# Optimization experiments

Measured on AMD Instinct MI355X. Metric: run time of the kernel, lower is better.

The kernel has to match this reference:

```python
import jax, jax.numpy as jnp
import numpy as np

NUM_HEADS = 16

def _apply_rope(t, cos, sin):
    # t: [B, nh, S, hd]; cos/sin: [S, hd//2]
    t1 = t[..., 0::2]
    t2 = t[..., 1::2]
    c = cos[None, None, :, :]
    s = sin[None, None, :, :]
    r1 = t1 * c - t2 * s
    r2 = t1 * s + t2 * c
    # interleave back to [..., hd]
    out = jnp.stack([r1, r2], axis=-1)
    return out.reshape(t.shape)

def setup_inputs() -> dict:
    key = jax.random.key(0)
    ks = jax.random.split(key, 6)
    B, S, H = 1, 4096, 1024
    hd = H // NUM_HEADS
    x = jax.random.normal(ks[0], (B, S, H), dtype=jnp.float32)
    # RoPE angle matrix: theta[pos, i] = pos / 10000^(2i/hd), shape [context, hd//2]
    pos = jnp.arange(S, dtype=jnp.float32)[:, None]
    inv_freq = 1.0 / (10000.0 ** (jnp.arange(0, hd, 2, dtype=jnp.float32) / hd))
    rotation = pos * inv_freq[None, :]
    sc = 1.0 / np.sqrt(H)
    W_qkv = jax.random.normal(ks[1], (H, 3 * H), dtype=jnp.float32) * sc
    b_qkv = jax.random.normal(ks[2], (3 * H,), dtype=jnp.float32) * 0.01
    W_out = jax.random.normal(ks[3], (H, H), dtype=jnp.float32) * sc
    b_out = jax.random.normal(ks[4], (H,), dtype=jnp.float32) * 0.01
    return {"x": x, "rotation": rotation, "W_qkv": W_qkv, "b_qkv": b_qkv,
            "W_out": W_out, "b_out": b_out, "window_size": 33}

def reference(x, rotation, W_qkv, b_qkv, W_out, b_out, window_size):
    B, S, H = x.shape
    nh = NUM_HEADS
    hd = H // nh
    W = window_size
    pad = W // 2
    qkv = x @ W_qkv + b_qkv                               # [B, S, 3H]
    qkv = qkv.reshape(B, S, nh, 3 * hd).transpose(0, 2, 1, 3)  # [B, nh, S, 3hd]
    q, k, v = jnp.split(qkv, 3, axis=-1)                  # each [B, nh, S, hd]
    cos = jnp.cos(rotation[:S])
    sin = jnp.sin(rotation[:S])
    q = _apply_rope(q, cos, sin)
    k = _apply_rope(k, cos, sin)
    # zero-pad along sequence, then gather sliding windows
    k_pad = jnp.pad(k, ((0, 0), (0, 0), (pad, pad), (0, 0)))
    v_pad = jnp.pad(v, ((0, 0), (0, 0), (pad, pad), (0, 0)))
    idx = jnp.arange(S)[:, None] + jnp.arange(W)[None, :]  # [S, W]
    k_win = k_pad[:, :, idx, :]                            # [B, nh, S, W, hd]
    v_win = v_pad[:, :, idx, :]
    scores = jnp.einsum('bnsh,bnswh->bnsw', q, k_win) / np.sqrt(hd)
    attn = jax.nn.softmax(scores, axis=-1)
    ctx = jnp.einsum('bnsw,bnswh->bnsh', attn, v_win)      # [B, nh, S, hd]
    ctx = ctx.transpose(0, 2, 1, 3).reshape(B, S, H)
    return ctx @ W_out + b_out
```

## Files before the change

kernel.cpp:

```cpp
#include <hip/hip_runtime.h>
#include <hip/hip_bf16.h>

#define S_LEN 4096
#define NH 16
#define HD 64
#define WIN 33
#define PAD 16
#define QT 64
#define KROWS 96
#define KPITCH_U 36

typedef short short8 __attribute__((ext_vector_type(8)));
typedef float f32x4 __attribute__((ext_vector_type(4)));

__device__ __forceinline__ float bl(unsigned u){ return __uint_as_float(u << 16); }
__device__ __forceinline__ float bh(unsigned u){ return __uint_as_float(u & 0xffff0000u); }
__device__ __forceinline__ unsigned f2bfu(float f){
  unsigned u = __float_as_uint(f);
  return (u + 0x7fffu + ((u >> 16) & 1u)) >> 16;
}
__device__ __forceinline__ unsigned pack2(float a, float b){ return f2bfu(a) | (f2bfu(b) << 16); }

__device__ __forceinline__ void gload_lds16(const void* g, void* l){
  __builtin_amdgcn_global_load_lds(
      (const __attribute__((address_space(1))) void*)g,
      (__attribute__((address_space(3))) void*)l, 16, 0, 0);
}


__global__ __launch_bounds__(256) void prep_all(
    const float* __restrict__ rot, float2* __restrict__ csq,
    const float* __restrict__ x, __hip_bfloat16* __restrict__ xb,
    const float* __restrict__ Wq, __hip_bfloat16* __restrict__ Wt1,
    const float* __restrict__ Wo, __hip_bfloat16* __restrict__ Wt2,
    const float* __restrict__ b_out, float* __restrict__ out)
{
  __shared__ float tile[32][33];
  const int b = blockIdx.x, tid = threadIdx.x;
  if (b < 512) {
    int t = b * 256 + tid;
    float v = rot[t], sv, cv;
    __sincosf(v, &sv, &cv);
    csq[t] = make_float2(cv, sv);
  } else if (b < 2560) {
    int t = (b - 512) * 256 + tid;
    const float4* p = (const float4*)x + (size_t)t * 2;
    float4 a = p[0], c = p[1];
    uint4 o;
    o.x = pack2(a.x, a.y); o.y = pack2(a.z, a.w);
    o.z = pack2(c.x, c.y); o.w = pack2(c.z, c.w);
    ((uint4*)xb)[t] = o;
  } else if (b < 6656) {
    const float* in; unsigned short* outp; int R, C, bx, by;
    if (b < 5632) { int bb = b - 2560; in = Wq; outp = (unsigned short*)Wt1; R = 1024; C = 3072; bx = bb % 96; by = bb / 96; }
    else          { int bb = b - 5632; in = Wo; outp = (unsigned short*)Wt2; R = 1024; C = 1024; bx = bb % 32; by = bb / 32; }
    int c0 = bx * 32, r0 = by * 32;
    int tx = tid & 31, ty = tid >> 5;
    #pragma unroll
    for (int i = 0; i < 4; ++i) {
      int r = ty + i * 8;
      tile[r][tx] = in[(size_t)(r0 + r) * C + c0 + tx];
    }
    __syncthreads();
    #pragma unroll
    for (int i = 0; i < 4; ++i) {
      int cc = ty + i * 8;
      outp[(size_t)(c0 + cc) * R + r0 + tx] = (unsigned short)f2bfu(tile[tx][cc]);
    }
  } else {
    int t = (b - 6656) * 256 + tid;
    const int cn = (t * 4) & 1023;
    ((float4*)out)[t] = *(const float4*)(b_out + cn);
  }
}


__global__ __launch_bounds__(256, 4) void gemm_qkv_rope(
    const __hip_bfloat16* __restrict__ A,
    const __hip_bfloat16* __restrict__ Bt,
    const float* __restrict__ bias,
    const float2* __restrict__ csq,
    unsigned short* __restrict__ Cout,
    int M, int N, int K)
{
  __shared__ unsigned int lA[128 * 64 / 2];
  __shared__ unsigned int lB[96 * 64 / 2];
  const int tid = threadIdx.x;
  const int wave = tid >> 6, lane = tid & 63;
  const int m0 = blockIdx.y * 128, n0 = blockIdx.x * 96;
  const int wm = (wave >> 1) * 64, wn = (wave & 1) * 48;
  const int l16 = lane >> 4, l15 = lane & 15;

  f32x4 acc[4][3];
  #pragma unroll
  for (int i = 0; i < 4; ++i)
    #pragma unroll
    for (int j = 0; j < 3; ++j) acc[i][j] = (f32x4){0.f, 0.f, 0.f, 0.f};

  const int nkt = K / 64;
  for (int kt = 0; kt < nkt; ++kt) {
    __syncthreads();
    #pragma unroll
    for (int it = 0; it < 4; ++it) {
      const int c = it * 256 + tid;
      const int r = c >> 3, s8 = c & 7;
      const int ss = s8 ^ (r & 7);
      gload_lds16(A + (size_t)(m0 + r) * K + kt * 64 + ss * 8, (char*)lA + c * 16);
    }
    #pragma unroll
    for (int it = 0; it < 3; ++it) {
      const int c = it * 256 + tid;
      const int r = c >> 3, s8 = c & 7;
      const int ss = s8 ^ (r & 7);
      gload_lds16(Bt + (size_t)(n0 + r) * K + kt * 64 + ss * 8, (char*)lB + c * 16);
    }
    __syncthreads();
    #pragma unroll
    for (int ks = 0; ks < 2; ++ks) {
      short8 af[4], bfr[3];
      #pragma unroll
      for (int mi = 0; mi < 4; ++mi) {
        const int r = wm + mi * 16 + l15;
        const int slot = (ks * 4 + l16) ^ (r & 7);
        uint4 u = *(const uint4*)((const char*)lA + r * 128 + slot * 16);
        af[mi] = __builtin_bit_cast(short8, u);
      }
      #pragma unroll
      for (int ni = 0; ni < 3; ++ni) {
        const int r = wn + ni * 16 + l15;
        const int slot = (ks * 4 + l16) ^ (r & 7);
        uint4 u = *(const uint4*)((const char*)lB + r * 128 + slot * 16);
        bfr[ni] = __builtin_bit_cast(short8, u);
      }
      #pragma unroll
      for (int mi = 0; mi < 4; ++mi)
        #pragma unroll
        for (int ni = 0; ni < 3; ++ni)
          acc[mi][ni] = __builtin_amdgcn_mfma_f32_16x16x32_bf16(af[mi], bfr[ni], acc[mi][ni], 0, 0, 0);
    }
  }

  #pragma unroll
  for (int ni = 0; ni < 3; ++ni) {
    const int cn = n0 + wn + ni * 16 + l15;
    const int rseg = cn % 192;
    const float bv = bias[cn];
    if (rseg < 128) {
      const int i = (rseg & 63) >> 1;
      const float sgn = (cn & 1) ? 1.f : -1.f;
      #pragma unroll
      for (int mi = 0; mi < 4; ++mi) {
        #pragma unroll
        for (int j = 0; j < 4; ++j) {
          const int rm = m0 + wm + mi * 16 + l16 * 4 + j;
          const float v = acc[mi][ni][j] + bv;
          const float p = __shfl_xor(v, 1);
          const float2 cs = csq[rm * 32 + i];
          Cout[(size_t)rm * N + cn] = (unsigned short)f2bfu(v * cs.x + p * (sgn * cs.y));
        }
      }
    } else {
      #pragma unroll
      for (int mi = 0; mi < 4; ++mi) {
        #pragma unroll
        for (int j = 0; j < 4; ++j) {
          const int rm = m0 + wm + mi * 16 + l16 * 4 + j;
          Cout[(size_t)rm * N + cn] = (unsigned short)f2bfu(acc[mi][ni][j] + bv);
        }
      }
    }
  }
}


__global__ __launch_bounds__(256, 4) void gemm_out_split(
    const __hip_bfloat16* __restrict__ A,
    const __hip_bfloat16* __restrict__ Bt,
    float* __restrict__ Cout,
    int M, int N, int K)
{
  __shared__ unsigned int lA[128 * 64 / 2];
  __shared__ unsigned int lB[64 * 64 / 2];
  const int tid = threadIdx.x;
  const int wave = tid >> 6, lane = tid & 63;
  const int m0 = blockIdx.y * 128, n0 = blockIdx.x * 64;
  const int k0 = blockIdx.z * (K >> 1);
  const int wm = (wave >> 1) * 64, wn = (wave & 1) * 32;
  const int l16 = lane >> 4, l15 = lane & 15;

  f32x4 acc[4][2];
  #pragma unroll
  for (int i = 0; i < 4; ++i)
    #pragma unroll
    for (int j = 0; j < 2; ++j) acc[i][j] = (f32x4){0.f, 0.f, 0.f, 0.f};

  const int nkt = (K >> 1) / 64;
  for (int kt = 0; kt < nkt; ++kt) {
    __syncthreads();
    #pragma unroll
    for (int it = 0; it < 4; ++it) {
      const int c = it * 256 + tid;
      const int r = c >> 3, s8 = c & 7;
      const int ss = s8 ^ (r & 7);
      gload_lds16(A + (size_t)(m0 + r) * K + k0 + kt * 64 + ss * 8, (char*)lA + c * 16);
    }
    #pragma unroll
    for (int it = 0; it < 2; ++it) {
      const int c = it * 256 + tid;
      const int r = c >> 3, s8 = c & 7;
      const int ss = s8 ^ (r & 7);
      gload_lds16(Bt + (size_t)(n0 + r) * K + k0 + kt * 64 + ss * 8, (char*)lB + c * 16);
    }
    __syncthreads();
    #pragma unroll
    for (int ks = 0; ks < 2; ++ks) {
      short8 af[4], bfr[2];
      #pragma unroll
      for (int mi = 0; mi < 4; ++mi) {
        const int r = wm + mi * 16 + l15;
        const int slot = (ks * 4 + l16) ^ (r & 7);
        uint4 u = *(const uint4*)((const char*)lA + r * 128 + slot * 16);
        af[mi] = __builtin_bit_cast(short8, u);
      }
      #pragma unroll
      for (int ni = 0; ni < 2; ++ni) {
        const int r = wn + ni * 16 + l15;
        const int slot = (ks * 4 + l16) ^ (r & 7);
        uint4 u = *(const uint4*)((const char*)lB + r * 128 + slot * 16);
        bfr[ni] = __builtin_bit_cast(short8, u);
      }
      #pragma unroll
      for (int mi = 0; mi < 4; ++mi)
        #pragma unroll
        for (int ni = 0; ni < 2; ++ni)
          acc[mi][ni] = __builtin_amdgcn_mfma_f32_16x16x32_bf16(af[mi], bfr[ni], acc[mi][ni], 0, 0, 0);
    }
  }

  #pragma unroll
  for (int ni = 0; ni < 2; ++ni) {
    const int cn = n0 + wn + ni * 16 + l15;
    #pragma unroll
    for (int mi = 0; mi < 4; ++mi) {
      #pragma unroll
      for (int j = 0; j < 4; ++j) {
        const int rm = m0 + wm + mi * 16 + l16 * 4 + j;
        atomicAdd(&Cout[(size_t)rm * N + cn], acc[mi][ni][j]);
      }
    }
  }
}


__global__ __launch_bounds__(256) void attn_kernel(const __hip_bfloat16* __restrict__ qkv,
                                                   __hip_bfloat16* __restrict__ ctx){
  __shared__ unsigned int kbuf[KROWS * KPITCH_U];
  __shared__ unsigned int vbuf[KROWS * KPITCH_U];
  const int tid = threadIdx.x;
  const int h   = blockIdx.x & 15;
  const int qs0 = (blockIdx.x >> 4) * QT;

  #pragma unroll
  for (int it = 0; it < 3; ++it) {
    int c = tid + it * 256;
    int r = c >> 3, s8 = c & 7;
    int srow = qs0 - PAD + r;
    uint4 kv = make_uint4(0, 0, 0, 0), vv = make_uint4(0, 0, 0, 0);
    if ((unsigned)srow < (unsigned)S_LEN) {
      kv = ((const uint4*)(qkv + (size_t)srow * 3072 + h * 192 + 64))[s8];
      vv = ((const uint4*)(qkv + (size_t)srow * 3072 + h * 192 + 128))[s8];
    }
    *(uint4*)(kbuf + r * KPITCH_U + s8 * 4) = kv;
    *(uint4*)(vbuf + r * KPITCH_U + s8 * 4) = vv;
  }

  const int ql = tid >> 2, t4 = tid & 3;
  const uint4* qp = (const uint4*)(qkv + (size_t)(qs0 + ql) * 3072 + h * 192);
  float qf[64];
  #pragma unroll
  for (int c = 0; c < 8; ++c) {
    uint4 v = qp[c];
    qf[c*8+0] = bl(v.x); qf[c*8+1] = bh(v.x);
    qf[c*8+2] = bl(v.y); qf[c*8+3] = bh(v.y);
    qf[c*8+4] = bl(v.z); qf[c*8+5] = bh(v.z);
    qf[c*8+6] = bl(v.w); qf[c*8+7] = bh(v.w);
  }
  __syncthreads();

  float sc[9];
  #pragma unroll
  for (int j = 0; j < 9; ++j) sc[j] = 0.f;
  float mx = -1e30f;
  #pragma unroll
  for (int j = 0; j < 9; ++j) {
    int w = t4 + 4 * j;
    if (w < WIN) {
      int rw = ql + w;
      const uint4* kp = (const uint4*)(kbuf + rw * KPITCH_U);
      float d = 0.f;
      #pragma unroll
      for (int c = 0; c < 8; ++c) {
        uint4 kv = kp[c];
        d += qf[c*8+0]*bl(kv.x) + qf[c*8+1]*bh(kv.x)
           + qf[c*8+2]*bl(kv.y) + qf[c*8+3]*bh(kv.y)
           + qf[c*8+4]*bl(kv.z) + qf[c*8+5]*bh(kv.z)
           + qf[c*8+6]*bl(kv.w) + qf[c*8+7]*bh(kv.w);
      }
      sc[j] = d * 0.125f;
      mx = fmaxf(mx, sc[j]);
    }
  }
  mx = fmaxf(mx, __shfl_xor(mx, 1));
  mx = fmaxf(mx, __shfl_xor(mx, 2));
  float sum = 0.f;
  #pragma unroll
  for (int j = 0; j < 9; ++j) {
    int w = t4 + 4 * j;
    if (w < WIN) { sc[j] = __expf(sc[j] - mx); sum += sc[j]; }
  }
  sum += __shfl_xor(sum, 1);
  sum += __shfl_xor(sum, 2);
  const float inv = 1.0f / sum;
  #pragma unroll
  for (int j = 0; j < 9; ++j) sc[j] *= inv;

  float accd[16];
  #pragma unroll
  for (int i = 0; i < 16; ++i) accd[i] = 0.f;
  #pragma unroll
  for (int w = 0; w < WIN; ++w) {
    float wgt = __shfl(sc[w >> 2], ((tid & 63) & ~3) | (w & 3), 64);
    int rw = ql + w;
    const uint4* vp = (const uint4*)(vbuf + rw * KPITCH_U + t4 * 8);
    uint4 a = vp[0], b = vp[1];
    float vf[16];
    vf[0]=bl(a.x); vf[1]=bh(a.x); vf[2]=bl(a.y); vf[3]=bh(a.y);
    vf[4]=bl(a.z); vf[5]=bh(a.z); vf[6]=bl(a.w); vf[7]=bh(a.w);
    vf[8]=bl(b.x); vf[9]=bh(b.x); vf[10]=bl(b.y); vf[11]=bh(b.y);
    vf[12]=bl(b.z); vf[13]=bh(b.z); vf[14]=bl(b.w); vf[15]=bh(b.w);
    #pragma unroll
    for (int i = 0; i < 16; ++i) accd[i] += wgt * vf[i];
  }

  unsigned short* op = (unsigned short*)ctx + (size_t)(qs0 + ql) * 1024 + h * 64 + t4 * 16;
  uint4 o1, o2;
  o1.x = pack2(accd[0], accd[1]);  o1.y = pack2(accd[2], accd[3]);
  o1.z = pack2(accd[4], accd[5]);  o1.w = pack2(accd[6], accd[7]);
  o2.x = pack2(accd[8], accd[9]);  o2.y = pack2(accd[10], accd[11]);
  o2.z = pack2(accd[12], accd[13]); o2.w = pack2(accd[14], accd[15]);
  *(uint4*)op = o1;
  *((uint4*)op + 1) = o2;
}


extern "C" void kernel_launch(void* const* d_in, const int* in_sizes, int n_in,
                              void* d_out, int out_size, void* d_ws, size_t ws_size,
                              hipStream_t stream)
{
  const float* x     = (const float*)d_in[0];
  const float* rot   = (const float*)d_in[1];
  const float* W_qkv = (const float*)d_in[2];
  const float* b_qkv = (const float*)d_in[3];
  const float* W_out = (const float*)d_in[4];
  const float* b_out = (const float*)d_in[5];
  float* out = (float*)d_out;

  char* ws = (char*)d_ws;
  __hip_bfloat16* xb   = (__hip_bfloat16*)(ws + 0);
  __hip_bfloat16* Wt1  = (__hip_bfloat16*)(ws + 8388608);
  __hip_bfloat16* Wt2  = (__hip_bfloat16*)(ws + 14680064);
  __hip_bfloat16* qkvb = (__hip_bfloat16*)(ws + 16777216);
  __hip_bfloat16* ctx  = (__hip_bfloat16*)(ws + 41943040);
  float2* csq          = (float2*)(ws + 50331648);

  prep_all<<<10752, 256, 0, stream>>>(rot, csq, x, xb, W_qkv, Wt1, W_out, Wt2, b_out, out);
  gemm_qkv_rope<<<dim3(3072 / 96, 4096 / 128), 256, 0, stream>>>(xb, Wt1, b_qkv, csq,
                                                                 (unsigned short*)qkvb, 4096, 3072, 1024);
  attn_kernel<<<64 * 16, 256, 0, stream>>>(qkvb, ctx);
  gemm_out_split<<<dim3(1024 / 64, 4096 / 128, 2), 256, 0, stream>>>(ctx, Wt2, out, 4096, 1024, 1024);
}
```

Before: 106.9 us.

## Replace split-K atomic output GEMM with 64x64 tiles and fused bias store

The output projection GEMM now runs as a full-K kernel on 64x64 tiles instead of a split-K-by-2 kernel on 128x64 tiles that accumulated into output with float atomics. The same grid size (1024 blocks) is kept. Bias is added in the epilogue with plain stores, so the prep kernel no longer pre-fills the output with bias. This removes the atomic traffic and the extra output initialization pass, but each block now loops over twice as many K steps and reuses less data per tile.

After: 87.29 us. 1.23x faster.

```diff
diff --git a/kernel.cpp b/kernel.cpp
--- a/kernel.cpp
+++ b/kernel.cpp
@@ -32,8 +32,7 @@
     const float* __restrict__ rot, float2* __restrict__ csq,
     const float* __restrict__ x, __hip_bfloat16* __restrict__ xb,
     const float* __restrict__ Wq, __hip_bfloat16* __restrict__ Wt1,
-    const float* __restrict__ Wo, __hip_bfloat16* __restrict__ Wt2,
-    const float* __restrict__ b_out, float* __restrict__ out)
+    const float* __restrict__ Wo, __hip_bfloat16* __restrict__ Wt2)
 {
   __shared__ float tile[32][33];
   const int b = blockIdx.x, tid = threadIdx.x;
@@ -50,10 +49,10 @@
     o.x = pack2(a.x, a.y); o.y = pack2(a.z, a.w);
     o.z = pack2(c.x, c.y); o.w = pack2(c.z, c.w);
     ((uint4*)xb)[t] = o;
-  } else if (b < 6656) {
-    const float* in; unsigned short* outp; int R, C, bx, by;
-    if (b < 5632) { int bb = b - 2560; in = Wq; outp = (unsigned short*)Wt1; R = 1024; C = 3072; bx = bb % 96; by = bb / 96; }
-    else          { int bb = b - 5632; in = Wo; outp = (unsigned short*)Wt2; R = 1024; C = 1024; bx = bb % 32; by = bb / 32; }
+  } else {
+    const float* in; unsigned short* out; int R, C, bx, by;
+    if (b < 5632) { int bb = b - 2560; in = Wq; out = (unsigned short*)Wt1; R = 1024; C = 3072; bx = bb % 96; by = bb / 96; }
+    else          { int bb = b - 5632; in = Wo; out = (unsigned short*)Wt2; R = 1024; C = 1024; bx = bb % 32; by = bb / 32; }
     int c0 = bx * 32, r0 = by * 32;
     int tx = tid & 31, ty = tid >> 5;
     #pragma unroll
@@ -65,12 +64,8 @@
     #pragma unroll
     for (int i = 0; i < 4; ++i) {
       int cc = ty + i * 8;
-      outp[(size_t)(c0 + cc) * R + r0 + tx] = (unsigned short)f2bfu(tile[tx][cc]);
-    }
-  } else {
-    int t = (b - 6656) * 256 + tid;
-    const int cn = (t * 4) & 1023;
-    ((float4*)out)[t] = *(const float4*)(b_out + cn);
+      out[(size_t)(c0 + cc) * R + r0 + tx] = (unsigned short)f2bfu(tile[tx][cc]);
+    }
   }
 }
 
@@ -173,50 +168,50 @@
 }
 
 
-__global__ __launch_bounds__(256, 4) void gemm_out_split(
+__global__ __launch_bounds__(256, 4) void gemm_out64(
     const __hip_bfloat16* __restrict__ A,
     const __hip_bfloat16* __restrict__ Bt,
+    const float* __restrict__ bias,
     float* __restrict__ Cout,
     int M, int N, int K)
 {
-  __shared__ unsigned int lA[128 * 64 / 2];
+  __shared__ unsigned int lA[64 * 64 / 2];
   __shared__ unsigned int lB[64 * 64 / 2];
   const int tid = threadIdx.x;
   const int wave = tid >> 6, lane = tid & 63;
-  const int m0 = blockIdx.y * 128, n0 = blockIdx.x * 64;
-  const int k0 = blockIdx.z * (K >> 1);
-  const int wm = (wave >> 1) * 64, wn = (wave & 1) * 32;
+  const int m0 = blockIdx.y * 64, n0 = blockIdx.x * 64;
+  const int wm = (wave >> 1) * 32, wn = (wave & 1) * 32;
   const int l16 = lane >> 4, l15 = lane & 15;
 
-  f32x4 acc[4][2];
-  #pragma unroll
-  for (int i = 0; i < 4; ++i)
+  f32x4 acc[2][2];
+  #pragma unroll
+  for (int i = 0; i < 2; ++i)
     #pragma unroll
     for (int j = 0; j < 2; ++j) acc[i][j] = (f32x4){0.f, 0.f, 0.f, 0.f};
 
-  const int nkt = (K >> 1) / 64;
+  const int nkt = K / 64;
   for (int kt = 0; kt < nkt; ++kt) {
     __syncthreads();
-    #pragma unroll
-    for (int it = 0; it < 4; ++it) {
-      const int c = it * 256 + tid;
-      const int r = c >> 3, s8 = c & 7;
-      const int ss = s8 ^ (r & 7);
-      gload_lds16(A + (size_t)(m0 + r) * K + k0 + kt * 64 + ss * 8, (char*)lA + c * 16);
-    }
     #pragma unroll
     for (int it = 0; it < 2; ++it) {
       const int c = it * 256 + tid;
       const int r = c >> 3, s8 = c & 7;
       const int ss = s8 ^ (r & 7);
-      gload_lds16(Bt + (size_t)(n0 + r) * K + k0 + kt * 64 + ss * 8, (char*)lB + c * 16);
+      gload_lds16(A + (size_t)(m0 + r) * K + kt * 64 + ss * 8, (char*)lA + c * 16);
+    }
+    #pragma unroll
+    for (int it = 0; it < 2; ++it) {
+      const int c = it * 256 + tid;
+      const int r = c >> 3, s8 = c & 7;
+      const int ss = s8 ^ (r & 7);
+      gload_lds16(Bt + (size_t)(n0 + r) * K + kt * 64 + ss * 8, (char*)lB + c * 16);
     }
     __syncthreads();
     #pragma unroll
     for (int ks = 0; ks < 2; ++ks) {
-      short8 af[4], bfr[2];
-      #pragma unroll
-      for (int mi = 0; mi < 4; ++mi) {
+      short8 af[2], bfr[2];
+      #pragma unroll
+      for (int mi = 0; mi < 2; ++mi) {
         const int r = wm + mi * 16 + l15;
         const int slot = (ks * 4 + l16) ^ (r & 7);
         uint4 u = *(const uint4*)((const char*)lA + r * 128 + slot * 16);
@@ -230,7 +225,7 @@
         bfr[ni] = __builtin_bit_cast(short8, u);
       }
       #pragma unroll
-      for (int mi = 0; mi < 4; ++mi)
+      for (int mi = 0; mi < 2; ++mi)
         #pragma unroll
         for (int ni = 0; ni < 2; ++ni)
           acc[mi][ni] = __builtin_amdgcn_mfma_f32_16x16x32_bf16(af[mi], bfr[ni], acc[mi][ni], 0, 0, 0);
@@ -240,12 +235,13 @@
   #pragma unroll
   for (int ni = 0; ni < 2; ++ni) {
     const int cn = n0 + wn + ni * 16 + l15;
-    #pragma unroll
-    for (int mi = 0; mi < 4; ++mi) {
+    const float bv = bias[cn];
+    #pragma unroll
+    for (int mi = 0; mi < 2; ++mi) {
       #pragma unroll
       for (int j = 0; j < 4; ++j) {
         const int rm = m0 + wm + mi * 16 + l16 * 4 + j;
-        atomicAdd(&Cout[(size_t)rm * N + cn], acc[mi][ni][j]);
+        Cout[(size_t)rm * N + cn] = acc[mi][ni][j] + bv;
       }
     }
   }
@@ -373,9 +369,9 @@
   __hip_bfloat16* ctx  = (__hip_bfloat16*)(ws + 41943040);
   float2* csq          = (float2*)(ws + 50331648);
 
-  prep_all<<<10752, 256, 0, stream>>>(rot, csq, x, xb, W_qkv, Wt1, W_out, Wt2, b_out, out);
+  prep_all<<<6656, 256, 0, stream>>>(rot, csq, x, xb, W_qkv, Wt1, W_out, Wt2);
   gemm_qkv_rope<<<dim3(3072 / 96, 4096 / 128), 256, 0, stream>>>(xb, Wt1, b_qkv, csq,
                                                                  (unsigned short*)qkvb, 4096, 3072, 1024);
   attn_kernel<<<64 * 16, 256, 0, stream>>>(qkvb, ctx);
-  gemm_out_split<<<dim3(1024 / 64, 4096 / 128, 2), 256, 0, stream>>>(ctx, Wt2, out, 4096, 1024, 1024);
-}
+  gemm_out64<<<dim3(1024 / 64, 4096 / 64), 256, 0, stream>>>(ctx, Wt2, b_out, out, 4096, 1024, 1024);
+}
```
